# Kernel optimization log

Hardware: AMD Instinct MI355X
Metric: run time of the kernel (lower is better)

## Reference

```python
import jax, jax.numpy as jnp
import numpy as np

N = 40000
E = 640000
D_IN = 128
D_HID = 128
N_CLS = 40


def setup_inputs() -> dict:
    key = jax.random.key(0)
    ks = jax.random.split(key, 12)
    x = jax.random.normal(ks[0], (N, D_IN), dtype=jnp.float32)
    edge_index = jax.random.randint(ks[1], (2, E), 0, N, dtype=jnp.int32)
    s = 1.0 / np.sqrt(D_IN)
    sh = 1.0 / np.sqrt(D_HID)
    sc = 1.0 / np.sqrt(4 * D_HID)
    # per-layer params: lin weight [out,in], combine weight [out, 4*out], bias [out]
    W0 = jax.random.uniform(ks[2], (D_HID, D_IN), jnp.float32, -s, s)
    C0 = jax.random.uniform(ks[3], (D_HID, 4 * D_HID), jnp.float32, -sc, sc)
    b0 = jnp.zeros((D_HID,), jnp.float32)
    W1 = jax.random.uniform(ks[4], (D_HID, D_HID), jnp.float32, -sh, sh)
    C1 = jax.random.uniform(ks[5], (D_HID, 4 * D_HID), jnp.float32, -sc, sc)
    b1 = jnp.zeros((D_HID,), jnp.float32)
    Wout = jax.random.uniform(ks[6], (N_CLS, D_HID), jnp.float32, -sh, sh)
    bout = jax.random.uniform(ks[7], (N_CLS,), jnp.float32, -sh, sh)
    return {"x": x, "edge_index": edge_index, "W0": W0, "C0": C0, "b0": b0,
            "W1": W1, "C1": C1, "b1": b1, "Wout": Wout, "bout": bout}


def _gcn_layer(x, row, col, W, C, b):
    n = x.shape[0]
    h = x @ W.T  # [N, H]
    ones = jnp.ones(row.shape, x.dtype)
    deg = jax.ops.segment_sum(ones, col, num_segments=n)  # in-degree incl. self-loops
    dinv = jnp.where(deg > 0, deg ** -0.5, 0.0)
    norm = dinv[row] * dinv[col]  # [E]
    msg = norm[:, None] * h[row]  # gather + scale, [E, H]
    add = jax.ops.segment_sum(msg, col, num_segments=n)
    mean = add / jnp.maximum(deg, 1.0)[:, None]
    mn = jax.ops.segment_min(msg, col, num_segments=n)
    mx = jax.ops.segment_max(msg, col, num_segments=n)
    out = jnp.concatenate([mean, add, mn, mx], axis=-1) @ C.T  # [N, H]
    return out + b


def reference(x, edge_index, W0, C0, b0, W1, C1, b1, Wout, bout):
    n = x.shape[0]
    loops = jnp.arange(n, dtype=edge_index.dtype)
    row = jnp.concatenate([edge_index[0], loops])
    col = jnp.concatenate([edge_index[1], loops])
    h = jax.nn.relu(_gcn_layer(x, row, col, W0, C0, b0))
    h = jax.nn.relu(_gcn_layer(h, row, col, W1, C1, b1))
    logits = h @ Wout.T + bout
    return jax.nn.log_softmax(logits, axis=-1)
```

## Files before the change

kernel.cpp:

```cpp
#include <hip/hip_runtime.h>
#include <hip/hip_fp16.h>
#include <math.h>

#define NN 40000
#define NE 640000
#define D 128
#define NCLS 40
#define CAP 48

typedef _Float16 f16x8 __attribute__((ext_vector_type(8)));
typedef float    f32x4 __attribute__((ext_vector_type(4)));

static inline int cdiv(int a, int b){ return (a + b - 1) / b; }

__global__ __launch_bounds__(256) void k_prep(int* __restrict__ cnt,
    const float* __restrict__ W0, _Float16* __restrict__ w0h,
    const float* __restrict__ C0, _Float16* __restrict__ c0h,
    const float* __restrict__ W1, _Float16* __restrict__ w1h,
    const float* __restrict__ C1, _Float16* __restrict__ c1h,
    const float* __restrict__ WO, _Float16* __restrict__ oh) {
  int i = blockIdx.x * 256 + threadIdx.x;
  if (i < NN) cnt[i] = 0;
  if (i < 16384) {
    float v = W0[i];
    int cc = i >> 7, k = i & 127;
    int pidx = (((cc >> 4) * 4 + (k >> 5)) * 64 + ((cc & 15) | (((k >> 3) & 3) << 4))) * 8 + (k & 7);
    w0h[pidx] = (_Float16)v;
  } else if (i < 81920) {
    int off = i - 16384;
    c0h[off] = (_Float16)C0[off];
  } else if (i < 98304) {
    int off = i - 81920;
    w1h[off] = (_Float16)W1[off];
  } else if (i < 163840) {
    int off = i - 98304;
    c1h[off] = (_Float16)C1[off];
  } else if (i < 168960) {
    int off = i - 163840;
    oh[off] = (_Float16)WO[off];
  }
}

__global__ __launch_bounds__(256) void k_fill(const int* __restrict__ row,
                                              const int* __restrict__ col,
                                              int* __restrict__ cnt,
                                              unsigned short* __restrict__ adj) {
  int i = blockIdx.x * 256 + threadIdx.x;
  if (i < NE) {
    int c = col[i];
    int s = atomicAdd(&cnt[c], 1);
    if (s < CAP) adj[c * CAP + s] = (unsigned short)row[i];
  }
}

__global__ __launch_bounds__(256) void k_dinvlin(const int* __restrict__ cnt,
                                                 float* __restrict__ dinv,
                                                 const float* __restrict__ A,
                                                 const _Float16* __restrict__ Wh,
                                                 _Float16* __restrict__ out) {
  if (blockIdx.x < 157) {
    int i = blockIdx.x * 256 + threadIdx.x;
    if (i < NN) dinv[i] = rsqrtf((float)(cnt[i] + 1));
    return;
  }
  __shared__ f16x8 Ah[64 * 8];
  int t = threadIdx.x;
  int lane = t & 63, wid = t >> 6;
  int wr = wid >> 1, wc = wid & 1;
  int row0 = (blockIdx.x - 157) * 64;

  f32x4 acc[2][4];
  #pragma unroll
  for (int m = 0; m < 2; m++)
    #pragma unroll
    for (int n = 0; n < 4; n++) acc[m][n] = (f32x4){0.f, 0.f, 0.f, 0.f};

  for (int k0 = 0; k0 < 128; k0 += 64) {
    __syncthreads();
    #pragma unroll
    for (int c = 0; c < 2; c++) {
      int id = t + c * 256;
      int r = id >> 3, q = id & 7;
      int ch = r * 8 + (q ^ (r & 7));
      const float* src = &A[(size_t)(row0 + r) * 128 + k0 + q * 8];
      float4 v0 = *(const float4*)src;
      float4 v1 = *(const float4*)(src + 4);
      float vv[8] = {v0.x, v0.y, v0.z, v0.w, v1.x, v1.y, v1.z, v1.w};
      f16x8 hi;
      #pragma unroll
      for (int j = 0; j < 8; j++) hi[j] = (_Float16)vv[j];
      Ah[ch] = hi;
    }
    __syncthreads();
    #pragma unroll
    for (int ks = 0; ks < 2; ks++) {
      int kchunk = (k0 >> 5) + ks;
      f16x8 ah[2], bh[4];
      #pragma unroll
      for (int m = 0; m < 2; m++) {
        int row = wr * 32 + m * 16 + (lane & 15);
        int ch = row * 8 + ((ks * 4 + (lane >> 4)) ^ (row & 7));
        ah[m] = Ah[ch];
      }
      #pragma unroll
      for (int n = 0; n < 4; n++) {
        int fidx = (((wc * 4 + n) * 4 + kchunk) * 64 + lane) * 8;
        bh[n] = *(const f16x8*)&Wh[fidx];
      }
      #pragma unroll
      for (int m = 0; m < 2; m++)
        #pragma unroll
        for (int n = 0; n < 4; n++)
          acc[m][n] = __builtin_amdgcn_mfma_f32_16x16x32_f16(ah[m], bh[n], acc[m][n], 0, 0, 0);
    }
  }

  #pragma unroll
  for (int m = 0; m < 2; m++) {
    int rbase = row0 + wr * 32 + m * 16 + (lane >> 4) * 4;
    float rs[4];
    #pragma unroll
    for (int j = 0; j < 4; j++) rs[j] = rsqrtf((float)(cnt[rbase + j] + 1));
    #pragma unroll
    for (int n = 0; n < 4; n++) {
      int col = wc * 64 + n * 16 + (lane & 15);
      #pragma unroll
      for (int j = 0; j < 4; j++)
        out[(size_t)(rbase + j) * 128 + col] = (_Float16)(acc[m][n][j] * rs[j]);
    }
  }
}

__global__ __launch_bounds__(256) void k_agg(const _Float16* __restrict__ hs,
                                             const int* __restrict__ cnt,
                                             const unsigned short* __restrict__ adj,
                                             const float* __restrict__ dinv,
                                             _Float16* __restrict__ agg) {
  int t = threadIdx.x;
  int g = t >> 4;
  int sl = t & 15;
  int nd = blockIdx.x * 16 + g;
  float di = dinv[nd];
  f16x8 sum = *(const f16x8*)&hs[(size_t)nd * D + sl * 8];
  f16x8 mn = sum, mx = sum;
  int ec = cnt[nd]; if (ec > CAP) ec = CAP;
  const unsigned short* abase = &adj[(size_t)nd * CAP];

  for (int eb = 0; eb < ec; eb += 16) {
    int rem = ec - eb; if (rem > 16) rem = 16;
    int re = abase[eb + (sl < rem ? sl : rem - 1)];
    int j = 0;
    for (; j + 8 <= rem; j += 8) {
      int r[8]; f16x8 v[8];
      #pragma unroll
      for (int u = 0; u < 8; u++) r[u] = __shfl(re, j + u, 16);
      #pragma unroll
      for (int u = 0; u < 8; u++) v[u] = *(const f16x8*)&hs[(size_t)r[u] * D + sl * 8];
      #pragma unroll
      for (int u = 0; u < 8; u++) {
        sum += v[u];
        mn = __builtin_elementwise_min(mn, v[u]);
        mx = __builtin_elementwise_max(mx, v[u]);
      }
    }
    for (; j + 4 <= rem; j += 4) {
      int r[4]; f16x8 v[4];
      #pragma unroll
      for (int u = 0; u < 4; u++) r[u] = __shfl(re, j + u, 16);
      #pragma unroll
      for (int u = 0; u < 4; u++) v[u] = *(const f16x8*)&hs[(size_t)r[u] * D + sl * 8];
      #pragma unroll
      for (int u = 0; u < 4; u++) {
        sum += v[u];
        mn = __builtin_elementwise_min(mn, v[u]);
        mx = __builtin_elementwise_max(mx, v[u]);
      }
    }
    for (; j < rem; j++) {
      int r0 = __shfl(re, j, 16);
      f16x8 v0 = *(const f16x8*)&hs[(size_t)r0 * D + sl * 8];
      sum += v0;
      mn = __builtin_elementwise_min(mn, v0);
      mx = __builtin_elementwise_max(mx, v0);
    }
  }

  _Float16 dh = (_Float16)di;
  f16x8 dv = {dh, dh, dh, dh, dh, dh, dh, dh};
  size_t base = (size_t)nd * 384 + sl * 8;
  *(f16x8*)&agg[base +   0] = sum * dv;
  *(f16x8*)&agg[base + 128] = mn  * dv;
  *(f16x8*)&agg[base + 256] = mx  * dv;
}

template<int MODE>
__global__ __launch_bounds__(256, 4) void k_comb(const _Float16* __restrict__ agg,
                                                 const float* __restrict__ dinv,
                                                 const _Float16* __restrict__ CW,
                                                 const float* __restrict__ bias,
                                                 const _Float16* __restrict__ W2h,
                                                 const float* __restrict__ bias2,
                                                 void* __restrict__ outv) {
  __shared__ f16x8 As[32 * 48];
  __shared__ f16x8 Bs[128 * 8];
  int t = threadIdx.x;
  int lane = t & 63, wid = t >> 6;
  int nd0 = blockIdx.x * 32;

  #pragma unroll
  for (int c = 0; c < 6; c++) {
    int id = t + c * 256;
    int r = id / 48, q = id - r * 48;
    As[r * 48 + (q ^ (r & 7))] = *(const f16x8*)&agg[(size_t)(nd0 + r) * 384 + q * 8];
  }

  f32x4 accA[2][2], accM[2][2];
  #pragma unroll
  for (int m = 0; m < 2; m++)
    #pragma unroll
    for (int n = 0; n < 2; n++) {
      accA[m][n] = (f32x4){0.f, 0.f, 0.f, 0.f};
      accM[m][n] = (f32x4){0.f, 0.f, 0.f, 0.f};
    }

  for (int k0 = 0; k0 < 512; k0 += 64) {
    __syncthreads();
    #pragma unroll
    for (int c = 0; c < 4; c++) {
      int id = t + c * 256;
      int cc = id >> 3, kq = id & 7;
      Bs[cc * 8 + (kq ^ (cc & 7))] = *(const f16x8*)&CW[(size_t)cc * 512 + k0 + kq * 8];
    }
    __syncthreads();
    int qbase = ((k0 < 256) ? (k0 & 127) : (k0 - 128)) >> 3;
    bool isMean = (k0 < 128);
    #pragma unroll
    for (int ks = 0; ks < 2; ks++) {
      f16x8 a[2], b[2];
      #pragma unroll
      for (int m = 0; m < 2; m++) {
        int row = m * 16 + (lane & 15);
        int qq = qbase + ks * 4 + (lane >> 4);
        a[m] = As[row * 48 + (qq ^ (row & 7))];
      }
      #pragma unroll
      for (int n = 0; n < 2; n++) {
        int cc = wid * 32 + n * 16 + (lane & 15);
        b[n] = Bs[cc * 8 + ((ks * 4 + (lane >> 4)) ^ (cc & 7))];
      }
      #pragma unroll
      for (int m = 0; m < 2; m++)
        #pragma unroll
        for (int n = 0; n < 2; n++) {
          if (isMean)
            accM[m][n] = __builtin_amdgcn_mfma_f32_16x16x32_f16(a[m], b[n], accM[m][n], 0, 0, 0);
          else
            accA[m][n] = __builtin_amdgcn_mfma_f32_16x16x32_f16(a[m], b[n], accA[m][n], 0, 0, 0);
        }
    }
  }

  __syncthreads();
  _Float16* A2 = (_Float16*)As;
  #pragma unroll
  for (int m = 0; m < 2; m++) {
    int lr0 = m * 16 + (lane >> 4) * 4;
    float d2[4];
    #pragma unroll
    for (int j = 0; j < 4; j++) {
      float dvv = dinv[nd0 + lr0 + j];
      d2[j] = dvv * dvv;
    }
    #pragma unroll
    for (int n = 0; n < 2; n++) {
      int cc = wid * 32 + n * 16 + (lane & 15);
      float bv = bias[cc];
      #pragma unroll
      for (int j = 0; j < 4; j++) {
        float v = fmaxf(accA[m][n][j] + d2[j] * accM[m][n][j] + bv, 0.f);
        int r = lr0 + j;
        A2[(r * 48 + 32 + ((cc >> 3) ^ (r & 7))) * 8 + (cc & 7)] = (_Float16)v;
      }
    }
  }

  if constexpr (MODE == 0) {
    f32x4 acc2[2][2];
    #pragma unroll
    for (int m = 0; m < 2; m++)
      #pragma unroll
      for (int n = 0; n < 2; n++) acc2[m][n] = (f32x4){0.f, 0.f, 0.f, 0.f};
    for (int k0 = 0; k0 < 128; k0 += 64) {
      __syncthreads();
      #pragma unroll
      for (int c = 0; c < 4; c++) {
        int id = t + c * 256;
        int cc = id >> 3, kq = id & 7;
        Bs[cc * 8 + (kq ^ (cc & 7))] = *(const f16x8*)&W2h[(size_t)cc * 128 + k0 + kq * 8];
      }
      __syncthreads();
      #pragma unroll
      for (int ks = 0; ks < 2; ks++) {
        int qq = (k0 >> 3) + ks * 4 + (lane >> 4);
        f16x8 a[2], b[2];
        #pragma unroll
        for (int m = 0; m < 2; m++) {
          int row = m * 16 + (lane & 15);
          a[m] = As[row * 48 + 32 + (qq ^ (row & 7))];
        }
        #pragma unroll
        for (int n = 0; n < 2; n++) {
          int cc = wid * 32 + n * 16 + (lane & 15);
          b[n] = Bs[cc * 8 + ((ks * 4 + (lane >> 4)) ^ (cc & 7))];
        }
        #pragma unroll
        for (int m = 0; m < 2; m++)
          #pragma unroll
          for (int n = 0; n < 2; n++)
            acc2[m][n] = __builtin_amdgcn_mfma_f32_16x16x32_f16(a[m], b[n], acc2[m][n], 0, 0, 0);
      }
    }
    _Float16* out = (_Float16*)outv;
    #pragma unroll
    for (int m = 0; m < 2; m++) {
      int rbase = nd0 + m * 16 + (lane >> 4) * 4;
      float rs[4];
      #pragma unroll
      for (int j = 0; j < 4; j++) rs[j] = dinv[rbase + j];
      #pragma unroll
      for (int n = 0; n < 2; n++) {
        int cc = wid * 32 + n * 16 + (lane & 15);
        #pragma unroll
        for (int j = 0; j < 4; j++)
          out[(size_t)(rbase + j) * 128 + cc] = (_Float16)(acc2[m][n][j] * rs[j]);
      }
    }
  } else {
    f32x4 acc3[3];
    #pragma unroll
    for (int n = 0; n < 3; n++) acc3[n] = (f32x4){0.f, 0.f, 0.f, 0.f};
    __syncthreads();
    #pragma unroll
    for (int c = 0; c < 3; c++) {
      int id = t + c * 256;
      int r = id >> 4, q = id & 15;
      f16x8 hv = {};
      if (r < NCLS) hv = *(const f16x8*)&W2h[(size_t)r * 128 + q * 8];
      Bs[r * 16 + (q ^ (r & 15))] = hv;
    }
    __syncthreads();
    if (wid < 2) {
      #pragma unroll
      for (int ks = 0; ks < 4; ks++) {
        int arow = wid * 16 + (lane & 15);
        f16x8 a = As[arow * 48 + 32 + ((ks * 4 + (lane >> 4)) ^ (arow & 7))];
        #pragma unroll
        for (int n = 0; n < 3; n++) {
          int br = n * 16 + (lane & 15);
          f16x8 b = Bs[br * 16 + ((ks * 4 + (lane >> 4)) ^ (br & 15))];
          acc3[n] = __builtin_amdgcn_mfma_f32_16x16x32_f16(a, b, acc3[n], 0, 0, 0);
        }
      }
      float* out = (float*)outv;
      int cl = lane & 15;
      float bb[3];
      #pragma unroll
      for (int n = 0; n < 3; n++) {
        int c = n * 16 + cl;
        bb[n] = (c < NCLS) ? bias2[c] : 0.f;
      }
      #pragma unroll
      for (int j = 0; j < 4; j++) {
        float v[3];
        #pragma unroll
        for (int n = 0; n < 3; n++) {
          int c = n * 16 + cl;
          v[n] = (c < NCLS) ? acc3[n][j] + bb[n] : -INFINITY;
        }
        float m = fmaxf(fmaxf(v[0], v[1]), v[2]);
        #pragma unroll
        for (int off = 1; off < 16; off <<= 1) m = fmaxf(m, __shfl_xor(m, off, 16));
        float s = 0.f;
        #pragma unroll
        for (int n = 0; n < 3; n++) {
          int c = n * 16 + cl;
          if (c < NCLS) s += expf(v[n] - m);
        }
        #pragma unroll
        for (int off = 1; off < 16; off <<= 1) s += __shfl_xor(s, off, 16);
        float ls = logf(s);
        int row = nd0 + wid * 16 + (lane >> 4) * 4 + j;
        #pragma unroll
        for (int n = 0; n < 3; n++) {
          int c = n * 16 + cl;
          if (c < NCLS) out[(size_t)row * NCLS + c] = v[n] - m - ls;
        }
      }
    }
  }
}

extern "C" void kernel_launch(void* const* d_in, const int* in_sizes, int n_in,
                              void* d_out, int out_size, void* d_ws, size_t ws_size,
                              hipStream_t stream) {
  const float* x    = (const float*)d_in[0];
  const int*   ei   = (const int*)  d_in[1];
  const float* W0   = (const float*)d_in[2];
  const float* C0   = (const float*)d_in[3];
  const float* b0   = (const float*)d_in[4];
  const float* W1   = (const float*)d_in[5];
  const float* C1   = (const float*)d_in[6];
  const float* b1   = (const float*)d_in[7];
  const float* Wout = (const float*)d_in[8];
  const float* bout = (const float*)d_in[9];
  float* out = (float*)d_out;

  char* ws = (char*)d_ws;
  size_t o = 0;
  auto take = [&](size_t bytes) -> char* {
    char* p = ws + o;
    o += (bytes + 255) & ~(size_t)255;
    return p;
  };
  int*            cnt    = (int*)           take((size_t)NN * 4);
  unsigned short* adj    = (unsigned short*)take((size_t)NN * CAP * 2);
  float*          dinv   = (float*)         take((size_t)NN * 4);
  _Float16*       W0h    = (_Float16*)      take(128 * 128 * 2);
  _Float16*       C0h    = (_Float16*)      take(128 * 512 * 2);
  _Float16*       W1h    = (_Float16*)      take(128 * 128 * 2);
  _Float16*       C1h    = (_Float16*)      take(128 * 512 * 2);
  _Float16*       Oh     = (_Float16*)      take(40 * 128 * 2);
  _Float16*       bufA   = (_Float16*)      take((size_t)NN * 128 * 2);
  _Float16*       bufB   = (_Float16*)      take((size_t)NN * 128 * 2);
  _Float16*       aggbuf = (_Float16*)      take((size_t)NN * 384 * 2);

  const int* row = ei;
  const int* col = ei + NE;

  k_prep<<<cdiv(168960, 256), 256, 0, stream>>>(cnt, W0, W0h, C0, C0h,
                                                W1, W1h, C1, C1h, Wout, Oh);
  k_fill<<<cdiv(NE, 256), 256, 0, stream>>>(row, col, cnt, adj);
  k_dinvlin<<<157 + 625, 256, 0, stream>>>(cnt, dinv, x, W0h, bufA);
  k_agg<<<2500, 256, 0, stream>>>(bufA, cnt, adj, dinv, aggbuf);
  k_comb<0><<<1250, 256, 0, stream>>>(aggbuf, dinv, C0h, b0, W1h, nullptr, bufB);
  k_agg<<<2500, 256, 0, stream>>>(bufB, cnt, adj, dinv, aggbuf);
  k_comb<1><<<1250, 256, 0, stream>>>(aggbuf, dinv, C1h, b1, Oh, bout, out);
}
```

Before: 145.6 us.

## Fuse adjacency fill with first linear layer and apply source norms in aggregation

The edge fill and the first dense transform now run as one launch, because the transform no longer needs degrees: the source-side normalization is applied during aggregation rather than pre-scaled into the features. Each aggregation thread computes rsqrt of the neighbor's degree, shuffles it across lanes, and scales each gathered row in fp16. The dinv buffer and a kernel launch go away, and the serial dependency between the fill and the linear layer is removed. In exchange, aggregation does an extra gather of neighbor counts and extra fp16 multiplies per edge.

```diff
diff --git a/kernel.cpp b/kernel.cpp
--- a/kernel.cpp
+++ b/kernel.cpp
@@ -41,33 +41,27 @@
   }
 }
 
-__global__ __launch_bounds__(256) void k_fill(const int* __restrict__ row,
-                                              const int* __restrict__ col,
-                                              int* __restrict__ cnt,
-                                              unsigned short* __restrict__ adj) {
-  int i = blockIdx.x * 256 + threadIdx.x;
-  if (i < NE) {
-    int c = col[i];
-    int s = atomicAdd(&cnt[c], 1);
-    if (s < CAP) adj[c * CAP + s] = (unsigned short)row[i];
-  }
-}
-
-__global__ __launch_bounds__(256) void k_dinvlin(const int* __restrict__ cnt,
-                                                 float* __restrict__ dinv,
-                                                 const float* __restrict__ A,
+__global__ __launch_bounds__(256) void k_filllin(const float* __restrict__ A,
                                                  const _Float16* __restrict__ Wh,
-                                                 _Float16* __restrict__ out) {
-  if (blockIdx.x < 157) {
-    int i = blockIdx.x * 256 + threadIdx.x;
-    if (i < NN) dinv[i] = rsqrtf((float)(cnt[i] + 1));
+                                                 _Float16* __restrict__ out,
+                                                 const int* __restrict__ row,
+                                                 const int* __restrict__ col,
+                                                 int* __restrict__ cnt,
+                                                 unsigned short* __restrict__ adj) {
+  if (blockIdx.x >= 625) {
+    int i = (blockIdx.x - 625) * 256 + threadIdx.x;
+    if (i < NE) {
+      int c = col[i];
+      int s = atomicAdd(&cnt[c], 1);
+      if (s < CAP) adj[c * CAP + s] = (unsigned short)row[i];
+    }
     return;
   }
   __shared__ f16x8 Ah[64 * 8];
   int t = threadIdx.x;
   int lane = t & 63, wid = t >> 6;
   int wr = wid >> 1, wc = wid & 1;
-  int row0 = (blockIdx.x - 157) * 64;
+  int row0 = blockIdx.x * 64;
 
   f32x4 acc[2][4];
   #pragma unroll
@@ -98,8 +92,8 @@
       f16x8 ah[2], bh[4];
       #pragma unroll
       for (int m = 0; m < 2; m++) {
-        int row = wr * 32 + m * 16 + (lane & 15);
-        int ch = row * 8 + ((ks * 4 + (lane >> 4)) ^ (row & 7));
+        int rr = wr * 32 + m * 16 + (lane & 15);
+        int ch = rr * 8 + ((ks * 4 + (lane >> 4)) ^ (rr & 7));
         ah[m] = Ah[ch];
       }
       #pragma unroll
@@ -118,75 +112,90 @@
   #pragma unroll
   for (int m = 0; m < 2; m++) {
     int rbase = row0 + wr * 32 + m * 16 + (lane >> 4) * 4;
-    float rs[4];
-    #pragma unroll
-    for (int j = 0; j < 4; j++) rs[j] = rsqrtf((float)(cnt[rbase + j] + 1));
     #pragma unroll
     for (int n = 0; n < 4; n++) {
-      int col = wc * 64 + n * 16 + (lane & 15);
+      int cc = wc * 64 + n * 16 + (lane & 15);
       #pragma unroll
       for (int j = 0; j < 4; j++)
-        out[(size_t)(rbase + j) * 128 + col] = (_Float16)(acc[m][n][j] * rs[j]);
+        out[(size_t)(rbase + j) * 128 + cc] = (_Float16)acc[m][n][j];
     }
   }
 }
 
-__global__ __launch_bounds__(256) void k_agg(const _Float16* __restrict__ hs,
+__global__ __launch_bounds__(256) void k_agg(const _Float16* __restrict__ h,
                                              const int* __restrict__ cnt,
                                              const unsigned short* __restrict__ adj,
-                                             const float* __restrict__ dinv,
                                              _Float16* __restrict__ agg) {
   int t = threadIdx.x;
   int g = t >> 4;
   int sl = t & 15;
   int nd = blockIdx.x * 16 + g;
-  float di = dinv[nd];
-  f16x8 sum = *(const f16x8*)&hs[(size_t)nd * D + sl * 8];
+  int ec0 = cnt[nd];
+  float di = rsqrtf((float)(ec0 + 1));
+  _Float16 dih = (_Float16)di;
+  f16x8 dv = {dih, dih, dih, dih, dih, dih, dih, dih};
+  f16x8 hv = *(const f16x8*)&h[(size_t)nd * D + sl * 8];
+  f16x8 sum = hv * dv;
   f16x8 mn = sum, mx = sum;
-  int ec = cnt[nd]; if (ec > CAP) ec = CAP;
+  int ec = ec0 > CAP ? CAP : ec0;
   const unsigned short* abase = &adj[(size_t)nd * CAP];
 
   for (int eb = 0; eb < ec; eb += 16) {
     int rem = ec - eb; if (rem > 16) rem = 16;
     int re = abase[eb + (sl < rem ? sl : rem - 1)];
+    float nsf = rsqrtf((float)(cnt[re] + 1));
     int j = 0;
     for (; j + 8 <= rem; j += 8) {
-      int r[8]; f16x8 v[8];
-      #pragma unroll
-      for (int u = 0; u < 8; u++) r[u] = __shfl(re, j + u, 16);
-      #pragma unroll
-      for (int u = 0; u < 8; u++) v[u] = *(const f16x8*)&hs[(size_t)r[u] * D + sl * 8];
+      int r[8]; float nf[8]; f16x8 v[8];
       #pragma unroll
       for (int u = 0; u < 8; u++) {
-        sum += v[u];
-        mn = __builtin_elementwise_min(mn, v[u]);
-        mx = __builtin_elementwise_max(mx, v[u]);
+        r[u]  = __shfl(re,  j + u, 16);
+        nf[u] = __shfl(nsf, j + u, 16);
+      }
+      #pragma unroll
+      for (int u = 0; u < 8; u++) v[u] = *(const f16x8*)&h[(size_t)r[u] * D + sl * 8];
+      #pragma unroll
+      for (int u = 0; u < 8; u++) {
+        _Float16 nh = (_Float16)nf[u];
+        f16x8 nv = {nh, nh, nh, nh, nh, nh, nh, nh};
+        f16x8 a = v[u] * nv;
+        sum += a;
+        mn = __builtin_elementwise_min(mn, a);
+        mx = __builtin_elementwise_max(mx, a);
       }
     }
     for (; j + 4 <= rem; j += 4) {
-      int r[4]; f16x8 v[4];
-      #pragma unroll
-      for (int u = 0; u < 4; u++) r[u] = __shfl(re, j + u, 16);
-      #pragma unroll
-      for (int u = 0; u < 4; u++) v[u] = *(const f16x8*)&hs[(size_t)r[u] * D + sl * 8];
+      int r[4]; float nf[4]; f16x8 v[4];
       #pragma unroll
       for (int u = 0; u < 4; u++) {
-        sum += v[u];
-        mn = __builtin_elementwise_min(mn, v[u]);
-        mx = __builtin_elementwise_max(mx, v[u]);
+        r[u]  = __shfl(re,  j + u, 16);
+        nf[u] = __shfl(nsf, j + u, 16);
+      }
+      #pragma unroll
+      for (int u = 0; u < 4; u++) v[u] = *(const f16x8*)&h[(size_t)r[u] * D + sl * 8];
+      #pragma unroll
+      for (int u = 0; u < 4; u++) {
+        _Float16 nh = (_Float16)nf[u];
+        f16x8 nv = {nh, nh, nh, nh, nh, nh, nh, nh};
+        f16x8 a = v[u] * nv;
+        sum += a;
+        mn = __builtin_elementwise_min(mn, a);
+        mx = __builtin_elementwise_max(mx, a);
       }
     }
     for (; j < rem; j++) {
       int r0 = __shfl(re, j, 16);
-      f16x8 v0 = *(const f16x8*)&hs[(size_t)r0 * D + sl * 8];
-      sum += v0;
-      mn = __builtin_elementwise_min(mn, v0);
-      mx = __builtin_elementwise_max(mx, v0);
-    }
-  }
-
-  _Float16 dh = (_Float16)di;
-  f16x8 dv = {dh, dh, dh, dh, dh, dh, dh, dh};
+      float n0 = __shfl(nsf, j, 16);
+      f16x8 v0 = *(const f16x8*)&h[(size_t)r0 * D + sl * 8];
+      _Float16 nh = (_Float16)n0;
+      f16x8 nv = {nh, nh, nh, nh, nh, nh, nh, nh};
+      f16x8 a = v0 * nv;
+      sum += a;
+      mn = __builtin_elementwise_min(mn, a);
+      mx = __builtin_elementwise_max(mx, a);
+    }
+  }
+
   size_t base = (size_t)nd * 384 + sl * 8;
   *(f16x8*)&agg[base +   0] = sum * dv;
   *(f16x8*)&agg[base + 128] = mn  * dv;
@@ -195,7 +204,7 @@
 
 template<int MODE>
 __global__ __launch_bounds__(256, 4) void k_comb(const _Float16* __restrict__ agg,
-                                                 const float* __restrict__ dinv,
+                                                 const int* __restrict__ cnt,
                                                  const _Float16* __restrict__ CW,
                                                  const float* __restrict__ bias,
                                                  const _Float16* __restrict__ W2h,
@@ -267,10 +276,8 @@
     int lr0 = m * 16 + (lane >> 4) * 4;
     float d2[4];
     #pragma unroll
-    for (int j = 0; j < 4; j++) {
-      float dvv = dinv[nd0 + lr0 + j];
-      d2[j] = dvv * dvv;
-    }
+    for (int j = 0; j < 4; j++)
+      d2[j] = 1.f / (float)(cnt[nd0 + lr0 + j] + 1);
     #pragma unroll
     for (int n = 0; n < 2; n++) {
       int cc = wid * 32 + n * 16 + (lane & 15);
@@ -324,15 +331,12 @@
     #pragma unroll
     for (int m = 0; m < 2; m++) {
       int rbase = nd0 + m * 16 + (lane >> 4) * 4;
-      float rs[4];
-      #pragma unroll
-      for (int j = 0; j < 4; j++) rs[j] = dinv[rbase + j];
       #pragma unroll
       for (int n = 0; n < 2; n++) {
         int cc = wid * 32 + n * 16 + (lane & 15);
         #pragma unroll
         for (int j = 0; j < 4; j++)
-          out[(size_t)(rbase + j) * 128 + cc] = (_Float16)(acc2[m][n][j] * rs[j]);
+          out[(size_t)(rbase + j) * 128 + cc] = (_Float16)acc2[m][n][j];
       }
     }
   } else {
@@ -424,7 +428,6 @@
   };
   int*            cnt    = (int*)           take((size_t)NN * 4);
   unsigned short* adj    = (unsigned short*)take((size_t)NN * CAP * 2);
-  float*          dinv   = (float*)         take((size_t)NN * 4);
   _Float16*       W0h    = (_Float16*)      take(128 * 128 * 2);
   _Float16*       C0h    = (_Float16*)      take(128 * 512 * 2);
   _Float16*       W1h    = (_Float16*)      take(128 * 128 * 2);
@@ -439,10 +442,9 @@
 
   k_prep<<<cdiv(168960, 256), 256, 0, stream>>>(cnt, W0, W0h, C0, C0h,
                                                 W1, W1h, C1, C1h, Wout, Oh);
-  k_fill<<<cdiv(NE, 256), 256, 0, stream>>>(row, col, cnt, adj);
-  k_dinvlin<<<157 + 625, 256, 0, stream>>>(cnt, dinv, x, W0h, bufA);
-  k_agg<<<2500, 256, 0, stream>>>(bufA, cnt, adj, dinv, aggbuf);
-  k_comb<0><<<1250, 256, 0, stream>>>(aggbuf, dinv, C0h, b0, W1h, nullptr, bufB);
-  k_agg<<<2500, 256, 0, stream>>>(bufB, cnt, adj, dinv, aggbuf);
-  k_comb<1><<<1250, 256, 0, stream>>>(aggbuf, dinv, C1h, b1, Oh, bout, out);
+  k_filllin<<<625 + 2500, 256, 0, stream>>>(x, W0h, bufA, row, col, cnt, adj);
+  k_agg<<<2500, 256, 0, stream>>>(bufA, cnt, adj, aggbuf);
+  k_comb<0><<<1250, 256, 0, stream>>>(aggbuf, cnt, C0h, b0, W1h, nullptr, bufB);
+  k_agg<<<2500, 256, 0, stream>>>(bufB, cnt, adj, aggbuf);
+  k_comb<1><<<1250, 256, 0, stream>>>(aggbuf, cnt, C1h, b1, Oh, bout, out);
 }
```

New measurement: 164.0 us. 1.13x slower.
